# Performance work log

Measured on AMD Instinct MI355X. Metric: run time of the kernel, lower is better.

Reference implementation:

```python
import jax, jax.numpy as jnp
import numpy as np

L = 6        # gnn_layers
H = 4        # heads
C = 128      # per-head channels = hidden // heads
HID = 512    # hidden
IN = 768     # in_dim
N = 20000    # nodes
E = 320000   # edges
P = 100000   # scored pairs


def _gelu(v):
    return jax.nn.gelu(v, approximate=False)


def _ln(v, g, b):
    m = v.mean(-1, keepdims=True)
    var = v.var(-1, keepdims=True)
    return (v - m) / jnp.sqrt(var + 1e-5) * g + b


def setup_inputs() -> dict:
    key = jax.random.key(0)
    ks = jax.random.split(key, 24)
    g = lambda k, shape, s=0.02: (jax.random.normal(k, shape, jnp.float32) * s)
    inp = {}
    inp["x"] = jax.random.normal(ks[0], (N, IN), jnp.float32)
    inp["edge_index"] = jax.random.randint(ks[1], (2, E), 0, N)
    inp["edges"] = jax.random.randint(ks[2], (2, P), 0, N)
    # FeatureMixer (no alt branch)
    inp["mixer_W"] = g(ks[3], (IN, HID)); inp["mixer_b"] = jnp.zeros((HID,), jnp.float32)
    # Stacked TransformerConv params per layer
    inp["Wq"] = g(ks[4], (L, HID, HID)); inp["bq"] = jnp.zeros((L, HID), jnp.float32)
    inp["Wk"] = g(ks[5], (L, HID, HID)); inp["bk"] = jnp.zeros((L, HID), jnp.float32)
    inp["Wv"] = g(ks[6], (L, HID, HID)); inp["bv"] = jnp.zeros((L, HID), jnp.float32)
    inp["Ws"] = g(ks[7], (L, HID, HID)); inp["bs"] = jnp.zeros((L, HID), jnp.float32)  # lin_skip (root weight)
    inp["ln_g"] = jnp.ones((L, HID), jnp.float32); inp["ln_b"] = jnp.zeros((L, HID), jnp.float32)
    # Dual projections
    inp["syn_W"] = g(ks[8], (HID, HID)); inp["syn_b"] = jnp.zeros((HID,), jnp.float32)
    inp["ant_W"] = g(ks[9], (HID, HID)); inp["ant_b"] = jnp.zeros((HID,), jnp.float32)
    # Bilinear score matrices
    inp["W_syn"] = g(ks[10], (HID, HID), 0.04)
    inp["W_ant"] = g(ks[11], (HID, HID), 0.04)
    # Gate MLP: Linear(4*HID, HID) -> GELU -> Linear(HID, 1) -> Sigmoid
    inp["gW1"] = g(ks[12], (4 * HID, HID)); inp["gb1"] = jnp.zeros((HID,), jnp.float32)
    inp["gW2"] = g(ks[13], (HID, 1)); inp["gb2"] = jnp.zeros((1,), jnp.float32)
    return inp


def reference(x, edge_index, edges, mixer_W, mixer_b, Wq, bq, Wk, bk, Wv, bv,
              Ws, bs, ln_g, ln_b, syn_W, syn_b, ant_W, ant_b, W_syn, W_ant,
              gW1, gb1, gW2, gb2):
    src, dst = edge_index[0], edge_index[1]
    scale = 1.0 / np.sqrt(C).astype(np.float32)
    # FeatureMixer (eval mode: dropout = identity)
    h = _gelu(x @ mixer_W + mixer_b)  # [N, HID]
    for l in range(L):
        # node-side projections, then gather per edge
        q = (h @ Wq[l] + bq[l]).reshape(N, H, C)
        k = (h @ Wk[l] + bk[l]).reshape(N, H, C)
        v = (h @ Wv[l] + bv[l]).reshape(N, H, C)
        logits = (q[dst] * k[src]).sum(-1) * scale          # [E, H]
        mx = jax.ops.segment_max(logits, dst, num_segments=N)   # [N, H]
        ex = jnp.exp(logits - mx[dst])
        den = jax.ops.segment_sum(ex, dst, num_segments=N)      # [N, H]
        alpha = ex / den[dst]                                   # segment softmax over incoming edges
        msg = alpha[..., None] * v[src]                         # [E, H, C]
        out = jax.ops.segment_sum(msg, dst, num_segments=N).reshape(N, HID)
        out = out + h @ Ws[l] + bs[l]                           # root/skip term of TransformerConv
        out = _gelu(out)
        h = _ln(h + out, ln_g[l], ln_b[l])
    z_syn = _gelu(h @ syn_W + syn_b)
    z_ant = _gelu(h @ ant_W + ant_b)
    i, j = edges[0], edges[1]
    vi_s, vj_s = z_syn[i], z_syn[j]
    vi_a, vj_a = z_ant[i], z_ant[j]
    s_syn = ((vi_s @ W_syn) * vj_s).sum(-1)
    s_ant = ((vi_a @ W_ant) * vj_a).sum(-1)
    pair = jnp.concatenate([jnp.abs(vi_s - vj_s), vi_s * vj_s,
                            jnp.abs(vi_a - vj_a), vi_a * vj_a], axis=-1)  # [P, 4*HID]
    g = jax.nn.sigmoid(_gelu(pair @ gW1 + gb1) @ gW2 + gb2).squeeze(-1)
    return g * s_ant + (1.0 - g) * (-s_syn)
```

## Files before the change

kernel.cpp:

```cpp
#include <hip/hip_runtime.h>
#include <cstdint>

#define L_LAYERS 6

typedef __attribute__((ext_vector_type(8))) short bf16x8;
typedef __attribute__((ext_vector_type(4))) float f32x4;
typedef __attribute__((ext_vector_type(2))) float f32x2;

__device__ __forceinline__ float gelu1(float v) {
    return 0.5f * v * (1.0f + erff(v * 0.7071067811865475f));
}

__device__ __forceinline__ unsigned int f2bf2(float a, float b) {
    union { float f; unsigned u; } x, y;
    x.f = a; y.f = b;
    unsigned lo = (x.u + 0x7FFFu + ((x.u >> 16) & 1u)) >> 16;
    unsigned hi = (y.u + 0x7FFFu + ((y.u >> 16) & 1u)) & 0xFFFF0000u;
    return lo | hi;
}

__device__ __forceinline__ unsigned short f2bf1(float a) {
    union { float f; unsigned u; } x;
    x.f = a;
    return (unsigned short)((x.u + 0x7FFFu + ((x.u >> 16) & 1u)) >> 16);
}

__device__ __forceinline__ unsigned cvt_pk_bf16(float lo, float hi) {
    unsigned r;
    asm("v_cvt_pk_bf16_f32 %0, %1, %2" : "=v"(r) : "v"(lo), "v"(hi));
    return r;
}

__device__ __forceinline__ float2 bfp2(unsigned u) {
    union { unsigned u; float f; } a, b;
    a.u = u << 16;
    b.u = u & 0xFFFF0000u;
    return make_float2(a.f, b.f);
}

__device__ __forceinline__ void gload16(const void* g, void* l) {
    __builtin_amdgcn_global_load_lds(
        (const __attribute__((address_space(1))) void*)g,
        (__attribute__((address_space(3))) void*)l, 16, 0, 0);
}


__global__ void k_zero(int* __restrict__ p, int n) {
    int i = blockIdx.x * 256 + threadIdx.x;
    if (i < n) p[i] = 0;
}

__global__ void k_cvt(const float* __restrict__ x, short* __restrict__ xb, int n8) {
    int i = blockIdx.x * 256 + threadIdx.x;
    if (i < n8) {
        const float4* p = (const float4*)(x + (size_t)i * 8);
        float4 a0 = p[0], a1 = p[1];
        uint4 o;
        o.x = f2bf2(a0.x, a0.y);
        o.y = f2bf2(a0.z, a0.w);
        o.z = f2bf2(a1.x, a1.y);
        o.w = f2bf2(a1.z, a1.w);
        *(uint4*)(xb + (size_t)i * 8) = o;
    }
}


__global__ void k_hist(const int* __restrict__ dst, int* __restrict__ hist, int E) {
    int e = blockIdx.x * 256 + threadIdx.x;
    if (e < E) atomicAdd(&hist[dst[e]], 1);
}

__global__ __launch_bounds__(1024) void k_scan(const int* __restrict__ hist,
                                               int* __restrict__ off, int n) {
    __shared__ int buf[1024];
    __shared__ int carry;
    int tid = threadIdx.x;
    if (tid == 0) carry = 0;
    __syncthreads();
    for (int base = 0; base < n; base += 1024) {
        int v = (base + tid < n) ? hist[base + tid] : 0;
        buf[tid] = v;
        __syncthreads();
        int x = v;
        for (int o = 1; o < 1024; o <<= 1) {
            int t = (tid >= o) ? buf[tid - o] : 0;
            __syncthreads();
            x += t;
            buf[tid] = x;
            __syncthreads();
        }
        int c = carry;
        if (base + tid < n) off[base + tid] = c + x - v;
        __syncthreads();
        if (tid == 1023) carry = c + buf[1023];
        __syncthreads();
    }
    if (tid == 0) off[n] = carry;
}

__global__ void k_scatter(const int* __restrict__ src, const int* __restrict__ dst,
                          const int* __restrict__ off, int* __restrict__ cursor,
                          int* __restrict__ srcS, int E) {
    int e = blockIdx.x * 256 + threadIdx.x;
    if (e < E) {
        int d = dst[e];
        int pos = off[d] + atomicAdd(&cursor[d], 1);
        srcS[pos] = src[e];
    }
}


__global__ void k_wcat(const float* __restrict__ Wq, const float* __restrict__ Wk,
                       const float* __restrict__ Wv, const float* __restrict__ Ws,
                       short* __restrict__ Wt) {
    int idx = blockIdx.x * 256 + threadIdx.x;
    int k = idx & 511;
    int nf = (idx >> 9) & 2047;
    int l = idx >> 20;
    int sel = nf >> 9, nn = nf & 511;
    const float* W = (sel == 0) ? Wq : (sel == 1) ? Wk : (sel == 2) ? Wv : Ws;
    float v = W[((size_t)l * 512 + k) * 512 + nn];
    Wt[idx] = (short)f2bf1(v);
}

__global__ void k_tr(const float* __restrict__ W, short* __restrict__ Wt, int K, int N,
                     int swz) {
    int k = blockIdx.x * 256 + threadIdx.x;
    int n = blockIdx.y;
    if (k < K) {
        int kk = k;
        if (swz) kk = (k & ~31) | (((((k >> 3) & 3) ^ ((n >> 1) & 3))) << 3) | (k & 7);
        Wt[(size_t)n * K + kk] = (short)f2bf1(W[(size_t)k * N + n]);
    }
}

__global__ void k_bcat(const float* __restrict__ bq, const float* __restrict__ bk,
                       const float* __restrict__ bv, const float* __restrict__ bs,
                       float* __restrict__ bcat) {
    int idx = blockIdx.x * 256 + threadIdx.x;
    if (idx >= L_LAYERS * 2048) return;
    int l = idx >> 11, n = idx & 2047;
    int sel = n >> 9, nn = n & 511;
    const float* b = (sel == 0) ? bq : (sel == 1) ? bk : (sel == 2) ? bv : bs;
    bcat[idx] = b[l * 512 + nn];
}

__global__ void k_bdual(const float* __restrict__ sb, const float* __restrict__ ab,
                        float* __restrict__ bd) {
    int idx = blockIdx.x * 256 + threadIdx.x;
    if (idx < 1024) bd[idx] = (idx < 512) ? sb[idx] : ab[idx - 512];
}


__global__ __launch_bounds__(256) void gemm_bb(
    const short* __restrict__ A, int lda,
    const short* __restrict__ Bt,
    const float* __restrict__ bias,
    short* __restrict__ C, unsigned char* __restrict__ C8, float* __restrict__ Cf,
    int ldc, int M, int N, int K, int act, int asel) {
    __shared__ __align__(16) short As[3 * 128 * 32];
    __shared__ __align__(16) short Bs[3 * 128 * 32];
    const int tid = threadIdx.x;
    const int lane = tid & 63;
    const int wave = tid >> 6;
    const int wr = (wave >> 1) * 64;
    const int wc = (wave & 1) * 64;
    const int l16 = lane & 15;
    const int quad = lane >> 4;
    const int row0 = blockIdx.x * 128;
    const int col0 = blockIdx.y * 128;
    const int c0 = tid, c1 = tid + 256;
    const int r0 = c0 >> 2, kq0 = (c0 & 3) * 8;
    const int r1 = c1 >> 2, kq1 = (c1 & 3) * 8;
    int ga0 = row0 + r0; if (ga0 >= M) ga0 = M - 1;
    int ga1 = row0 + r1; if (ga1 >= M) ga1 = M - 1;
    const short* Ab = A + (asel ? (col0 & 512) : 0);
    const short* Ap0 = Ab + (size_t)ga0 * lda + kq0;
    const short* Ap1 = Ab + (size_t)ga1 * lda + kq1;
    const short* Bp0 = Bt + (size_t)(col0 + r0) * K + kq0;
    const short* Bp1 = Bt + (size_t)(col0 + r1) * K + kq1;

    f32x4 acc[4][4];
#pragma unroll
    for (int i = 0; i < 4; ++i)
#pragma unroll
        for (int j = 0; j < 4; ++j)
            acc[i][j] = f32x4{0.f, 0.f, 0.f, 0.f};

    const int nsteps = K >> 5;
    gload16(Ap0, &As[c0 * 8]);
    gload16(Ap1, &As[c1 * 8]);
    gload16(Bp0, &Bs[c0 * 8]);
    gload16(Bp1, &Bs[c1 * 8]);
    gload16(Ap0 + 32, &As[4096 + c0 * 8]);
    gload16(Ap1 + 32, &As[4096 + c1 * 8]);
    gload16(Bp0 + 32, &Bs[4096 + c0 * 8]);
    gload16(Bp1 + 32, &Bs[4096 + c1 * 8]);
    int cur = 0, nx2 = 2;
#pragma unroll 1
    for (int ks = 0; ks < nsteps - 1; ++ks) {
        asm volatile("s_waitcnt vmcnt(4)" ::: "memory");
        __builtin_amdgcn_s_barrier();
        if (ks + 2 < nsteps) {
            const int kb = (ks + 2) * 32;
            const int nb = nx2 * 4096;
            gload16(Ap0 + kb, &As[nb + c0 * 8]);
            gload16(Ap1 + kb, &As[nb + c1 * 8]);
            gload16(Bp0 + kb, &Bs[nb + c0 * 8]);
            gload16(Bp1 + kb, &Bs[nb + c1 * 8]);
        }
        const int cb = cur * 4096;
        bf16x8 af[4], bfr[4];
#pragma unroll
        for (int i = 0; i < 4; ++i)
            af[i] = *(const bf16x8*)&As[cb + (wr + i * 16 + l16) * 32 + quad * 8];
#pragma unroll
        for (int j = 0; j < 4; ++j)
            bfr[j] = *(const bf16x8*)&Bs[cb + (wc + j * 16 + l16) * 32 + quad * 8];
#pragma unroll
        for (int i = 0; i < 4; ++i)
#pragma unroll
            for (int j = 0; j < 4; ++j)
                acc[i][j] = __builtin_amdgcn_mfma_f32_16x16x32_bf16(af[i], bfr[j], acc[i][j], 0, 0, 0);
        cur = (cur == 2) ? 0 : cur + 1;
        nx2 = (nx2 == 2) ? 0 : nx2 + 1;
    }
    {
        asm volatile("s_waitcnt vmcnt(0)" ::: "memory");
        __builtin_amdgcn_s_barrier();
        const int cb = cur * 4096;
        bf16x8 af[4], bfr[4];
#pragma unroll
        for (int i = 0; i < 4; ++i)
            af[i] = *(const bf16x8*)&As[cb + (wr + i * 16 + l16) * 32 + quad * 8];
#pragma unroll
        for (int j = 0; j < 4; ++j)
            bfr[j] = *(const bf16x8*)&Bs[cb + (wc + j * 16 + l16) * 32 + quad * 8];
#pragma unroll
        for (int i = 0; i < 4; ++i)
#pragma unroll
            for (int j = 0; j < 4; ++j)
                acc[i][j] = __builtin_amdgcn_mfma_f32_16x16x32_bf16(af[i], bfr[j], acc[i][j], 0, 0, 0);
    }
#pragma unroll
    for (int i = 0; i < 4; ++i) {
        int rbase = row0 + wr + i * 16 + quad * 4;
#pragma unroll
        for (int j = 0; j < 4; ++j) {
            int c = col0 + wc + j * 16 + l16;
            float bv = bias ? bias[c] : 0.0f;
#pragma unroll
            for (int rg = 0; rg < 4; ++rg) {
                int gr = rbase + rg;
                if (gr < M) {
                    float v = acc[i][j][rg] + bv;
                    if (act) v = gelu1(v);
                    C[(size_t)gr * ldc + c] = (short)f2bf1(v);
                    if (C8) {
                        int r8 = __builtin_amdgcn_cvt_pk_fp8_f32(v, v, 0, false);
                        C8[(size_t)gr * ldc + c] = (unsigned char)(r8 & 0xFF);
                    }
                    if (Cf) Cf[(size_t)gr * ldc + c] = v;
                }
            }
        }
    }
}


__global__ __launch_bounds__(256) void gemm_qkvs(
    const short* __restrict__ A,
    const short* __restrict__ Bt,
    const float* __restrict__ bias,
    short* __restrict__ qvs,
    unsigned char* __restrict__ kv8,
    int M, int mtiles) {
    const int K = 512;
    const int id = blockIdx.x;
    const int xcd = id & 7;
    const int t = id >> 3;
    const int col_t = t & 15;
    const int row_t = (t >> 4) * 8 + xcd;
    if (row_t >= mtiles) return;
    const int row0 = row_t * 128;
    const int col0 = col_t * 128;
    __shared__ __align__(16) short As[3 * 128 * 32];
    __shared__ __align__(16) short Bs[3 * 128 * 32];
    const int tid = threadIdx.x;
    const int lane = tid & 63;
    const int wave = tid >> 6;
    const int wr = (wave >> 1) * 64;
    const int wc = (wave & 1) * 64;
    const int l16 = lane & 15;
    const int quad = lane >> 4;
    const int c0 = tid, c1 = tid + 256;
    const int r0 = c0 >> 2, kq0 = (c0 & 3) * 8;
    const int r1 = c1 >> 2, kq1 = (c1 & 3) * 8;
    int ga0 = row0 + r0; if (ga0 >= M) ga0 = M - 1;
    int ga1 = row0 + r1; if (ga1 >= M) ga1 = M - 1;
    const short* Ap0 = A + (size_t)ga0 * K + kq0;
    const short* Ap1 = A + (size_t)ga1 * K + kq1;
    const short* Bp0 = Bt + (size_t)(col0 + r0) * K + kq0;
    const short* Bp1 = Bt + (size_t)(col0 + r1) * K + kq1;

    f32x4 acc[4][4];
#pragma unroll
    for (int i = 0; i < 4; ++i)
#pragma unroll
        for (int j = 0; j < 4; ++j)
            acc[i][j] = f32x4{0.f, 0.f, 0.f, 0.f};

    gload16(Ap0, &As[c0 * 8]);
    gload16(Ap1, &As[c1 * 8]);
    gload16(Bp0, &Bs[c0 * 8]);
    gload16(Bp1, &Bs[c1 * 8]);
    gload16(Ap0 + 32, &As[4096 + c0 * 8]);
    gload16(Ap1 + 32, &As[4096 + c1 * 8]);
    gload16(Bp0 + 32, &Bs[4096 + c0 * 8]);
    gload16(Bp1 + 32, &Bs[4096 + c1 * 8]);
    int cur = 0, nx2 = 2;
#pragma unroll 1
    for (int ks = 0; ks < 15; ++ks) {
        asm volatile("s_waitcnt vmcnt(4)" ::: "memory");
        __builtin_amdgcn_s_barrier();
        if (ks + 2 < 16) {
            const int kb = (ks + 2) * 32;
            const int nb = nx2 * 4096;
            gload16(Ap0 + kb, &As[nb + c0 * 8]);
            gload16(Ap1 + kb, &As[nb + c1 * 8]);
            gload16(Bp0 + kb, &Bs[nb + c0 * 8]);
            gload16(Bp1 + kb, &Bs[nb + c1 * 8]);
        }
        const int cb = cur * 4096;
        bf16x8 af[4], bfr[4];
#pragma unroll
        for (int i = 0; i < 4; ++i)
            af[i] = *(const bf16x8*)&As[cb + (wr + i * 16 + l16) * 32 + quad * 8];
#pragma unroll
        for (int j = 0; j < 4; ++j)
            bfr[j] = *(const bf16x8*)&Bs[cb + (wc + j * 16 + l16) * 32 + quad * 8];
#pragma unroll
        for (int i = 0; i < 4; ++i)
#pragma unroll
            for (int j = 0; j < 4; ++j)
                acc[i][j] = __builtin_amdgcn_mfma_f32_16x16x32_bf16(af[i], bfr[j], acc[i][j], 0, 0, 0);
        cur = (cur == 2) ? 0 : cur + 1;
        nx2 = (nx2 == 2) ? 0 : nx2 + 1;
    }
    {
        asm volatile("s_waitcnt vmcnt(0)" ::: "memory");
        __builtin_amdgcn_s_barrier();
        const int cb = cur * 4096;
        bf16x8 af[4], bfr[4];
#pragma unroll
        for (int i = 0; i < 4; ++i)
            af[i] = *(const bf16x8*)&As[cb + (wr + i * 16 + l16) * 32 + quad * 8];
#pragma unroll
        for (int j = 0; j < 4; ++j)
            bfr[j] = *(const bf16x8*)&Bs[cb + (wc + j * 16 + l16) * 32 + quad * 8];
#pragma unroll
        for (int i = 0; i < 4; ++i)
#pragma unroll
            for (int j = 0; j < 4; ++j)
                acc[i][j] = __builtin_amdgcn_mfma_f32_16x16x32_bf16(af[i], bfr[j], acc[i][j], 0, 0, 0);
    }
#pragma unroll
    for (int i = 0; i < 4; ++i) {
        int rbase = row0 + wr + i * 16 + quad * 4;
#pragma unroll
        for (int j = 0; j < 4; ++j) {
            int c = col0 + wc + j * 16 + l16;
            int sec = c >> 9;
            int cc = c & 511;
            float bv = bias[c];
#pragma unroll
            for (int rg = 0; rg < 4; ++rg) {
                int gr = rbase + rg;
                if (gr < M) {
                    float v = acc[i][j][rg] + bv;
                    if (sec == 1 || sec == 2) {
                        int r8 = __builtin_amdgcn_cvt_pk_fp8_f32(v, v, 0, false);
                        int off = (sec == 1) ? cc : 512 + cc;
                        kv8[(size_t)gr * 1024 + off] = (unsigned char)(r8 & 0xFF);
                    } else {
                        int off = (sec == 0) ? cc : 512 + cc;
                        qvs[(size_t)gr * 1024 + off] = (short)f2bf1(v);
                    }
                }
            }
        }
    }
}


__global__ __launch_bounds__(512, 2) void gemm_gate(
    const unsigned char* __restrict__ z8,
    const int* __restrict__ pi, const int* __restrict__ pj, int P,
    const short* __restrict__ Bt,
    const float* __restrict__ gb1,
    const float* __restrict__ gW2,
    const float* __restrict__ gb2,
    const float* __restrict__ ssyn,
    const float* __restrict__ sant,
    float* __restrict__ out) {
    __shared__ __align__(16) short Bab[2 * 512 * 32];
    __shared__ __align__(16) short Bmu[2 * 512 * 32];
    __shared__ __align__(16) short Asab[128 * 32];
    __shared__ __align__(16) short Asmu[128 * 32];
    __shared__ int iArr[128];
    __shared__ int jArr[128];
    __shared__ float rowsum[128];
    const int row0 = blockIdx.x * 128;
    const int tid = threadIdx.x;
    const int lane = tid & 63;
    const int wave = tid >> 6;
    const int wm = wave >> 2;
    const int wn = wave & 3;
    const int l16 = lane & 15;
    const int quad = lane >> 4;
    const int arow = tid >> 2;
    const int aslot = tid & 3;
    const int qs = (quad ^ ((l16 >> 1) & 3)) * 8;
    const int awoff = arow * 32 + ((aslot ^ ((arow >> 1) & 3)) << 3);

    if (tid < 128) {
        int p = row0 + tid;
        int ok = (p < P);
        iArr[tid] = ok ? pi[p] : 0;
        jArr[tid] = ok ? pj[p] : 0;
        rowsum[tid] = 0.0f;
    }
    __syncthreads();
    const unsigned char* zi = z8 + (size_t)iArr[arow] * 1024 + aslot * 8;
    const unsigned char* zj = z8 + (size_t)jArr[arow] * 1024 + aslot * 8;
    const short* brow = Bt + (size_t)(tid >> 2) * 2048 + (tid & 3) * 8;

    f32x4 acc[4][8];
#pragma unroll
    for (int i = 0; i < 4; ++i)
#pragma unroll
        for (int j = 0; j < 8; ++j)
            acc[i][j] = f32x4{0.f, 0.f, 0.f, 0.f};

    auto CHB = [](int kc) { return ((kc >> 4) << 10) + ((kc & 15) << 5); };
    auto KOFF = [](int kc) { return ((kc >> 4) << 9) + ((kc & 15) << 5); };
    auto STAGE = [&](int kc, int mu, short* buf) {
        const short* src = brow + CHB(kc) + (mu ? 512 : 0);
#pragma unroll
        for (int g = 0; g < 4; ++g)
            gload16(src + (size_t)(g * 128) * 2048, buf + (g * 512 + tid) * 8);
    };
    auto CVT = [&](uint2 xu, uint2 yu, uint4& aa, uint4& am) {
        f32x2 x0 = __builtin_amdgcn_cvt_pk_f32_fp8((int)xu.x, false);
        f32x2 x1 = __builtin_amdgcn_cvt_pk_f32_fp8((int)xu.x, true);
        f32x2 x2 = __builtin_amdgcn_cvt_pk_f32_fp8((int)xu.y, false);
        f32x2 x3 = __builtin_amdgcn_cvt_pk_f32_fp8((int)xu.y, true);
        f32x2 y0 = __builtin_amdgcn_cvt_pk_f32_fp8((int)yu.x, false);
        f32x2 y1 = __builtin_amdgcn_cvt_pk_f32_fp8((int)yu.x, true);
        f32x2 y2 = __builtin_amdgcn_cvt_pk_f32_fp8((int)yu.y, false);
        f32x2 y3 = __builtin_amdgcn_cvt_pk_f32_fp8((int)yu.y, true);
        aa.x = cvt_pk_bf16(fabsf(x0.x - y0.x), fabsf(x0.y - y0.y));
        aa.y = cvt_pk_bf16(fabsf(x1.x - y1.x), fabsf(x1.y - y1.y));
        aa.z = cvt_pk_bf16(fabsf(x2.x - y2.x), fabsf(x2.y - y2.y));
        aa.w = cvt_pk_bf16(fabsf(x3.x - y3.x), fabsf(x3.y - y3.y));
        am.x = cvt_pk_bf16(x0.x * y0.x, x0.y * y0.y);
        am.y = cvt_pk_bf16(x1.x * y1.x, x1.y * y1.y);
        am.z = cvt_pk_bf16(x2.x * y2.x, x2.y * y2.y);
        am.w = cvt_pk_bf16(x3.x * y3.x, x3.y * y3.y);
    };
    auto MFMA_PHASE = [&](const short* As, const short* Bp) {
        bf16x8 af[4];
#pragma unroll
        for (int i = 0; i < 4; ++i)
            af[i] = *(const bf16x8*)&As[(wm * 64 + i * 16 + l16) * 32 + qs];
#pragma unroll
        for (int j = 0; j < 8; ++j) {
            bf16x8 bf = *(const bf16x8*)&Bp[(wn * 128 + j * 16 + l16) * 32 + qs];
#pragma unroll
            for (int i = 0; i < 4; ++i)
                acc[i][j] = __builtin_amdgcn_mfma_f32_16x16x32_bf16(af[i], bf, acc[i][j], 0, 0, 0);
        }
    };

    STAGE(0, 0, Bab);
    uint2 xu = *(const uint2*)zi;
    uint2 yu = *(const uint2*)zj;
    uint4 aa, am, am_hold;
    CVT(xu, yu, aa, am);
    *(uint4*)&Asab[awoff] = aa;
    am_hold = am;

#pragma unroll 1
    for (int kc = 0; kc < 31; ++kc) {
        const int cur = kc & 1;
        STAGE(kc, 1, Bmu + cur * 16384);
        uint2 xn = *(const uint2*)(zi + KOFF(kc + 1));
        uint2 yn = *(const uint2*)(zj + KOFF(kc + 1));
        asm volatile("s_waitcnt vmcnt(6) lgkmcnt(0)" ::: "memory");
        __builtin_amdgcn_s_barrier();
        MFMA_PHASE(Asab, Bab + cur * 16384);
        *(uint4*)&Asmu[awoff] = am_hold;
        STAGE(kc + 1, 0, Bab + (cur ^ 1) * 16384);
        CVT(xn, yn, aa, am);
        asm volatile("s_waitcnt vmcnt(4) lgkmcnt(0)" ::: "memory");
        __builtin_amdgcn_s_barrier();
        MFMA_PHASE(Asmu, Bmu + cur * 16384);
        *(uint4*)&Asab[awoff] = aa;
        am_hold = am;
    }
    STAGE(31, 1, Bmu + 16384);
    asm volatile("s_waitcnt vmcnt(4) lgkmcnt(0)" ::: "memory");
    __builtin_amdgcn_s_barrier();
    MFMA_PHASE(Asab, Bab + 16384);
    *(uint4*)&Asmu[awoff] = am_hold;
    asm volatile("s_waitcnt vmcnt(0) lgkmcnt(0)" ::: "memory");
    __builtin_amdgcn_s_barrier();
    MFMA_PHASE(Asmu, Bmu + 16384);

#pragma unroll
    for (int i = 0; i < 4; ++i) {
#pragma unroll
        for (int rg = 0; rg < 4; ++rg) {
            float partial = 0.f;
#pragma unroll
            for (int j = 0; j < 8; ++j) {
                int cc = wn * 128 + j * 16 + l16;
                partial += gelu1(acc[i][j][rg] + gb1[cc]) * gW2[cc];
            }
            partial += __shfl_xor(partial, 1);
            partial += __shfl_xor(partial, 2);
            partial += __shfl_xor(partial, 4);
            partial += __shfl_xor(partial, 8);
            if (l16 == 0)
                atomicAdd(&rowsum[wm * 64 + i * 16 + quad * 4 + rg], partial);
        }
    }
    __syncthreads();
    if (tid < 128) {
        int p = row0 + tid;
        if (p < P) {
            float s = 1.0f / (1.0f + __expf(-(rowsum[tid] + gb2[0])));
            out[p] = s * sant[p] - (1.0f - s) * ssyn[p];
        }
    }
}


__global__ __launch_bounds__(256) void k_attn(const short* __restrict__ qvs,
                                              const unsigned char* __restrict__ kv8,
                                              const int* __restrict__ srcS,
                                              const int* __restrict__ offs,
                                              float* __restrict__ h,
                                              short* __restrict__ h_bf,
                                              const float* __restrict__ lng,
                                              const float* __restrict__ lnb, int Nn) {
    const int tid = threadIdx.x;
    const int lane = tid & 63;
    const int wv = tid >> 6;
    const int n = blockIdx.x * 4 + wv;
    if (n >= Nn) return;
    const int st = offs[n], en = offs[n + 1];
    const size_t chOff = (size_t)lane * 8;

    uint4 qv = *(const uint4*)(qvs + (size_t)n * 1024 + chOff);
    float2 q0 = bfp2(qv.x), q1 = bfp2(qv.y), q2 = bfp2(qv.z), q3 = bfp2(qv.w);
    float acc[8];
#pragma unroll
    for (int i = 0; i < 8; ++i) acc[i] = 0.f;
    float m_l = -3.4e38f, l_l = 0.f;

    auto PROC = [&](uint2 kq, uint2 vq) {
        f32x2 k0 = __builtin_amdgcn_cvt_pk_f32_fp8((int)kq.x, false);
        f32x2 k1 = __builtin_amdgcn_cvt_pk_f32_fp8((int)kq.x, true);
        f32x2 k2 = __builtin_amdgcn_cvt_pk_f32_fp8((int)kq.y, false);
        f32x2 k3 = __builtin_amdgcn_cvt_pk_f32_fp8((int)kq.y, true);
        float d = q0.x * k0.x + q0.y * k0.y + q1.x * k1.x + q1.y * k1.y +
                  q2.x * k2.x + q2.y * k2.y + q3.x * k3.x + q3.y * k3.y;
        d += __shfl_xor(d, 1);
        d += __shfl_xor(d, 2);
        d += __shfl_xor(d, 4);
        d += __shfl_xor(d, 8);
        float lg = d * 0.08838834764831845f;
        float m_new = fmaxf(m_l, lg);
        float sc = __expf(m_l - m_new);
        float p = __expf(lg - m_new);
        l_l = l_l * sc + p;
        m_l = m_new;
        f32x2 v0 = __builtin_amdgcn_cvt_pk_f32_fp8((int)vq.x, false);
        f32x2 v1 = __builtin_amdgcn_cvt_pk_f32_fp8((int)vq.x, true);
        f32x2 v2 = __builtin_amdgcn_cvt_pk_f32_fp8((int)vq.y, false);
        f32x2 v3 = __builtin_amdgcn_cvt_pk_f32_fp8((int)vq.y, true);
        acc[0] = acc[0] * sc + p * v0.x; acc[1] = acc[1] * sc + p * v0.y;
        acc[2] = acc[2] * sc + p * v1.x; acc[3] = acc[3] * sc + p * v1.y;
        acc[4] = acc[4] * sc + p * v2.x; acc[5] = acc[5] * sc + p * v2.y;
        acc[6] = acc[6] * sc + p * v3.x; acc[7] = acc[7] * sc + p * v3.y;
    };

    for (int e0 = st; e0 < en; e0 += 64) {
        int cnt = min(64, en - e0);
        int myS = (lane < cnt) ? srcS[e0 + lane] : 0;
        int ei = 0;
        for (; ei + 8 <= cnt; ei += 8) {
            const unsigned char* rp[8];
#pragma unroll
            for (int u = 0; u < 8; ++u) {
                int s = __shfl(myS, ei + u);
                rp[u] = kv8 + (size_t)s * 1024 + chOff;
            }
            uint2 kk[8], vv[8];
#pragma unroll
            for (int u = 0; u < 8; ++u) {
                kk[u] = *(const uint2*)rp[u];
                vv[u] = *(const uint2*)(rp[u] + 512);
            }
#pragma unroll
            for (int u = 0; u < 8; ++u) PROC(kk[u], vv[u]);
        }
        for (; ei < cnt; ++ei) {
            int s = __shfl(myS, ei);
            const unsigned char* srow = kv8 + (size_t)s * 1024 + chOff;
            uint2 kq = *(const uint2*)srow;
            uint2 vq = *(const uint2*)(srow + 512);
            PROC(kq, vq);
        }
    }
    float rinv = (en > st) ? 1.0f / l_l : 0.f;
    uint4 su = *(const uint4*)(qvs + (size_t)n * 1024 + 512 + chOff);
    float2 s0 = bfp2(su.x), s1 = bfp2(su.y), s2 = bfp2(su.z), s3 = bfp2(su.w);
    float sv[8] = {s0.x, s0.y, s1.x, s1.y, s2.x, s2.y, s3.x, s3.y};
    const float* hp = h + (size_t)n * 512 + chOff;
    float4 h0 = *(const float4*)hp;
    float4 h1 = *(const float4*)(hp + 4);
    float hv[8] = {h0.x, h0.y, h0.z, h0.w, h1.x, h1.y, h1.z, h1.w};
    float r[8];
    float sum = 0.f, ssq = 0.f;
#pragma unroll
    for (int i = 0; i < 8; ++i) {
        r[i] = hv[i] + gelu1(acc[i] * rinv + sv[i]);
        sum += r[i];
        ssq += r[i] * r[i];
    }
    for (int o = 32; o; o >>= 1) {
        sum += __shfl_xor(sum, o);
        ssq += __shfl_xor(ssq, o);
    }
    float mean = sum * (1.0f / 512.0f);
    float var = ssq * (1.0f / 512.0f) - mean * mean;
    float inv = rsqrtf(var + 1e-5f);
    const float* gp = lng + chOff;
    const float* bp = lnb + chOff;
    float4 g0 = *(const float4*)gp, g1 = *(const float4*)(gp + 4);
    float4 b0 = *(const float4*)bp, b1 = *(const float4*)(bp + 4);
    float ga[8] = {g0.x, g0.y, g0.z, g0.w, g1.x, g1.y, g1.z, g1.w};
    float ba[8] = {b0.x, b0.y, b0.z, b0.w, b1.x, b1.y, b1.z, b1.w};
    float o8[8];
#pragma unroll
    for (int i = 0; i < 8; ++i) o8[i] = (r[i] - mean) * inv * ga[i] + ba[i];
    float* hw = h + (size_t)n * 512 + chOff;
    *(float4*)hw = make_float4(o8[0], o8[1], o8[2], o8[3]);
    *(float4*)(hw + 4) = make_float4(o8[4], o8[5], o8[6], o8[7]);
    uint4 ob;
    ob.x = f2bf2(o8[0], o8[1]);
    ob.y = f2bf2(o8[2], o8[3]);
    ob.z = f2bf2(o8[4], o8[5]);
    ob.w = f2bf2(o8[6], o8[7]);
    *(uint4*)(h_bf + (size_t)n * 512 + chOff) = ob;
}


__global__ __launch_bounds__(256) void k_pairscore(const short* __restrict__ z,
                                                   const short* __restrict__ t,
                                                   const int* __restrict__ pi,
                                                   const int* __restrict__ pj,
                                                   float* __restrict__ ssyn,
                                                   float* __restrict__ sant, int P) {
    int p = blockIdx.x * 4 + (threadIdx.x >> 6);
    if (p >= P) return;
    int lane = threadIdx.x & 63;
    int i = pi[p], j = pj[p];
    uint4 a = *(const uint4*)(t + (size_t)i * 1024 + lane * 8);
    uint4 b = *(const uint4*)(z + (size_t)j * 1024 + lane * 8);
    float2 a0 = bfp2(a.x), a1 = bfp2(a.y), a2 = bfp2(a.z), a3 = bfp2(a.w);
    float2 b0 = bfp2(b.x), b1 = bfp2(b.y), b2 = bfp2(b.z), b3 = bfp2(b.w);
    float ds = a0.x * b0.x + a0.y * b0.y + a1.x * b1.x + a1.y * b1.y +
               a2.x * b2.x + a2.y * b2.y + a3.x * b3.x + a3.y * b3.y;
    uint4 c = *(const uint4*)(t + (size_t)i * 1024 + 512 + lane * 8);
    uint4 d = *(const uint4*)(z + (size_t)j * 1024 + 512 + lane * 8);
    float2 c0 = bfp2(c.x), c1 = bfp2(c.y), c2 = bfp2(c.z), c3 = bfp2(c.w);
    float2 d0 = bfp2(d.x), d1 = bfp2(d.y), d2 = bfp2(d.z), d3 = bfp2(d.w);
    float da = c0.x * d0.x + c0.y * d0.y + c1.x * d1.x + c1.y * d1.y +
               c2.x * d2.x + c2.y * d2.y + c3.x * d3.x + c3.y * d3.y;
    for (int o = 32; o; o >>= 1) {
        ds += __shfl_xor(ds, o);
        da += __shfl_xor(da, o);
    }
    if (lane == 0) { ssyn[p] = ds; sant[p] = da; }
}


extern "C" void kernel_launch(void* const* d_in, const int* in_sizes, int n_in,
                              void* d_out, int out_size, void* d_ws, size_t ws_size,
                              hipStream_t stream) {
    const float* x = (const float*)d_in[0];
    const int* ei = (const int*)d_in[1];
    const int* pe = (const int*)d_in[2];
    const float* mixer_W = (const float*)d_in[3];
    const float* mixer_b = (const float*)d_in[4];
    const float* Wq = (const float*)d_in[5];
    const float* bq = (const float*)d_in[6];
    const float* Wk = (const float*)d_in[7];
    const float* bk = (const float*)d_in[8];
    const float* Wv = (const float*)d_in[9];
    const float* bv = (const float*)d_in[10];
    const float* Ws = (const float*)d_in[11];
    const float* bs = (const float*)d_in[12];
    const float* ln_g = (const float*)d_in[13];
    const float* ln_b = (const float*)d_in[14];
    const float* syn_W = (const float*)d_in[15];
    const float* syn_b = (const float*)d_in[16];
    const float* ant_W = (const float*)d_in[17];
    const float* ant_b = (const float*)d_in[18];
    const float* W_syn = (const float*)d_in[19];
    const float* W_ant = (const float*)d_in[20];
    const float* gW1 = (const float*)d_in[21];
    const float* gb1 = (const float*)d_in[22];
    const float* gW2 = (const float*)d_in[23];
    const float* gb2 = (const float*)d_in[24];
    float* out = (float*)d_out;

    const int Nn = in_sizes[0] / 768;
    const int E = in_sizes[1] / 2;
    const int P = in_sizes[2] / 2;

    char* w = (char*)d_ws;
    auto alloc = [&](size_t bytes) -> char* {
        char* p = w;
        w += (bytes + 255) & ~(size_t)255;
        return p;
    };
    float* h = (float*)alloc((size_t)Nn * 512 * 4);
    short* h_bf = (short*)alloc((size_t)Nn * 512 * 2);
    char* U = alloc((size_t)Nn * 2048 * 2);
    short* x_bf = (short*)U;
    short* qvs = (short*)U;
    unsigned char* kv8 = (unsigned char*)(U + (size_t)Nn * 1024 * 2);
    short* zB = (short*)U;
    short* tB = (short*)(U + (size_t)Nn * 1024 * 2);
    unsigned char* z8 = (unsigned char*)alloc((size_t)Nn * 1024);
    float* ssyn = (float*)alloc((size_t)P * 2 * 4);
    float* sant = ssyn + P;
    int* srcS = (int*)alloc((size_t)E * 4);
    int* hist = (int*)alloc((size_t)Nn * 2 * 4);
    int* cursor = hist + Nn;
    int* offs = (int*)alloc((size_t)(Nn + 1) * 4);
    short* mixWt = (short*)alloc((size_t)512 * 768 * 2);
    short* wcat = (short*)alloc((size_t)L_LAYERS * 2048 * 512 * 2);
    short* dualWt = (short*)alloc((size_t)1024 * 512 * 2);
    short* bilWt = (short*)alloc((size_t)1024 * 512 * 2);
    short* gw1t = (short*)alloc((size_t)512 * 2048 * 2);
    float* bcat = (float*)alloc((size_t)L_LAYERS * 2048 * 4);
    float* bdual = (float*)alloc((size_t)1024 * 4);

    k_zero<<<(2 * Nn + 255) / 256, 256, 0, stream>>>(hist, 2 * Nn);
    k_hist<<<(E + 255) / 256, 256, 0, stream>>>(ei + E, hist, E);
    k_scan<<<1, 1024, 0, stream>>>(hist, offs, Nn);
    k_scatter<<<(E + 255) / 256, 256, 0, stream>>>(ei, ei + E, offs, cursor, srcS, E);

    k_wcat<<<(L_LAYERS * 2048 * 512) / 256, 256, 0, stream>>>(Wq, Wk, Wv, Ws, wcat);
    k_tr<<<dim3(3, 512), 256, 0, stream>>>(mixer_W, mixWt, 768, 512, 0);
    k_tr<<<dim3(2, 512), 256, 0, stream>>>(syn_W, dualWt, 512, 512, 0);
    k_tr<<<dim3(2, 512), 256, 0, stream>>>(ant_W, dualWt + 512 * 512, 512, 512, 0);
    k_tr<<<dim3(2, 512), 256, 0, stream>>>(W_syn, bilWt, 512, 512, 0);
    k_tr<<<dim3(2, 512), 256, 0, stream>>>(W_ant, bilWt + 512 * 512, 512, 512, 0);
    k_tr<<<dim3(8, 512), 256, 0, stream>>>(gW1, gw1t, 2048, 512, 1);
    k_bcat<<<48, 256, 0, stream>>>(bq, bk, bv, bs, bcat);
    k_bdual<<<4, 256, 0, stream>>>(syn_b, ant_b, bdual);

    const int mtiles = (Nn + 127) / 128;
    k_cvt<<<(Nn * 768 / 8 + 255) / 256, 256, 0, stream>>>(x, x_bf, Nn * 768 / 8);
    gemm_bb<<<dim3(mtiles, 4), 256, 0, stream>>>(x_bf, 768, mixWt, mixer_b, h_bf,
                                                 nullptr, h, 512, Nn, 512, 768, 1, 0);

    const int qk_grid = ((mtiles + 7) / 8) * 8 * 16;
    for (int l = 0; l < L_LAYERS; ++l) {
        gemm_qkvs<<<qk_grid, 256, 0, stream>>>(h_bf, wcat + (size_t)l * 2048 * 512,
                                               bcat + l * 2048, qvs, kv8, Nn, mtiles);
        k_attn<<<(Nn + 3) / 4, 256, 0, stream>>>(qvs, kv8, srcS, offs, h, h_bf,
                                                 ln_g + l * 512, ln_b + l * 512, Nn);
    }

    gemm_bb<<<dim3(mtiles, 8), 256, 0, stream>>>(h_bf, 512, dualWt, bdual, zB, z8,
                                                 nullptr, 1024, Nn, 1024, 512, 1, 0);
    gemm_bb<<<dim3(mtiles, 8), 256, 0, stream>>>(zB, 1024, bilWt, nullptr, tB, nullptr,
                                                 nullptr, 1024, Nn, 1024, 512, 0, 1);

    k_pairscore<<<(P + 3) / 4, 256, 0, stream>>>(zB, tB, pe, pe + P, ssyn, sant, P);

    const int ptiles2 = (P + 127) / 128;
    gemm_gate<<<ptiles2, 512, 0, stream>>>(z8, pe, pe + P, P, gw1t, gb1, gW2,
                                           gb2, ssyn, sant, out);
}
```

Baseline: 1.616 ms.

## Fuse bilinear pair scoring into the gate GEMM kernel

Removes the separate pair-score kernel and computes the syn and ant bilinear dot products inside the gate GEMM main loop. Each thread loads matching 8-element bf16 slices of tB[i] and zB[j] alongside the fp8 gathers, accumulates partial dots, and reduces them across the four threads of a row at the end. This drops a kernel launch and the round trip of the intermediate score arrays through global memory, and lets the gathers overlap MFMA work. In exchange it adds two vector loads per K-step to the gate loop's memory pipeline and retunes the wait counts, which could stall the B-tile staging.

Measured after the change: 1.598 ms. About the same (-1.1%).

```diff
diff --git a/kernel.cpp b/kernel.cpp
--- a/kernel.cpp
+++ b/kernel.cpp
@@ -400,8 +400,8 @@
     const float* __restrict__ gb1,
     const float* __restrict__ gW2,
     const float* __restrict__ gb2,
-    const float* __restrict__ ssyn,
-    const float* __restrict__ sant,
+    const short* __restrict__ tB,
+    const short* __restrict__ zB,
     float* __restrict__ out) {
     __shared__ __align__(16) short Bab[2 * 512 * 32];
     __shared__ __align__(16) short Bmu[2 * 512 * 32];
@@ -410,6 +410,8 @@
     __shared__ int iArr[128];
     __shared__ int jArr[128];
     __shared__ float rowsum[128];
+    __shared__ float dsS[128];
+    __shared__ float daS[128];
     const int row0 = blockIdx.x * 128;
     const int tid = threadIdx.x;
     const int lane = tid & 63;
@@ -433,6 +435,8 @@
     __syncthreads();
     const unsigned char* zi = z8 + (size_t)iArr[arow] * 1024 + aslot * 8;
     const unsigned char* zj = z8 + (size_t)jArr[arow] * 1024 + aslot * 8;
+    const short* tbi = tB + (size_t)iArr[arow] * 1024 + aslot * 8;
+    const short* zbj = zB + (size_t)jArr[arow] * 1024 + aslot * 8;
     const short* brow = Bt + (size_t)(tid >> 2) * 2048 + (tid & 3) * 8;
 
     f32x4 acc[4][8];
@@ -468,6 +472,12 @@
         am.z = cvt_pk_bf16(x2.x * y2.x, x2.y * y2.y);
         am.w = cvt_pk_bf16(x3.x * y3.x, x3.y * y3.y);
     };
+    auto DOT8 = [&](uint4 tv, uint4 zv) -> float {
+        float2 t0 = bfp2(tv.x), t1 = bfp2(tv.y), t2 = bfp2(tv.z), t3 = bfp2(tv.w);
+        float2 p0 = bfp2(zv.x), p1 = bfp2(zv.y), p2 = bfp2(zv.z), p3 = bfp2(zv.w);
+        return t0.x * p0.x + t0.y * p0.y + t1.x * p1.x + t1.y * p1.y +
+               t2.x * p2.x + t2.y * p2.y + t3.x * p3.x + t3.y * p3.y;
+    };
     auto MFMA_PHASE = [&](const short* As, const short* Bp) {
         bf16x8 af[4];
 #pragma unroll
@@ -485,10 +495,13 @@
     STAGE(0, 0, Bab);
     uint2 xu = *(const uint2*)zi;
     uint2 yu = *(const uint2*)zj;
+    uint4 tu = *(const uint4*)tbi;
+    uint4 zu = *(const uint4*)zbj;
     uint4 aa, am, am_hold;
     CVT(xu, yu, aa, am);
     *(uint4*)&Asab[awoff] = aa;
     am_hold = am;
+    float ds = 0.f, da = 0.f;
 
 #pragma unroll 1
     for (int kc = 0; kc < 31; ++kc) {
@@ -496,19 +509,26 @@
         STAGE(kc, 1, Bmu + cur * 16384);
         uint2 xn = *(const uint2*)(zi + KOFF(kc + 1));
         uint2 yn = *(const uint2*)(zj + KOFF(kc + 1));
+        {
+            float pd = DOT8(tu, zu);
+            if (kc < 16) ds += pd; else da += pd;
+        }
         asm volatile("s_waitcnt vmcnt(6) lgkmcnt(0)" ::: "memory");
         __builtin_amdgcn_s_barrier();
         MFMA_PHASE(Asab, Bab + cur * 16384);
         *(uint4*)&Asmu[awoff] = am_hold;
         STAGE(kc + 1, 0, Bab + (cur ^ 1) * 16384);
+        tu = *(const uint4*)(tbi + KOFF(kc + 1));
+        zu = *(const uint4*)(zbj + KOFF(kc + 1));
         CVT(xn, yn, aa, am);
-        asm volatile("s_waitcnt vmcnt(4) lgkmcnt(0)" ::: "memory");
+        asm volatile("s_waitcnt vmcnt(6) lgkmcnt(0)" ::: "memory");
         __builtin_amdgcn_s_barrier();
         MFMA_PHASE(Asmu, Bmu + cur * 16384);
         *(uint4*)&Asab[awoff] = aa;
         am_hold = am;
     }
     STAGE(31, 1, Bmu + 16384);
+    da += DOT8(tu, zu);
     asm volatile("s_waitcnt vmcnt(4) lgkmcnt(0)" ::: "memory");
     __builtin_amdgcn_s_barrier();
     MFMA_PHASE(Asab, Bab + 16384);
@@ -516,6 +536,12 @@
     asm volatile("s_waitcnt vmcnt(0) lgkmcnt(0)" ::: "memory");
     __builtin_amdgcn_s_barrier();
     MFMA_PHASE(Asmu, Bmu + 16384);
+
+    ds += __shfl_xor(ds, 1);
+    ds += __shfl_xor(ds, 2);
+    da += __shfl_xor(da, 1);
+    da += __shfl_xor(da, 2);
+    if (aslot == 0) { dsS[arow] = ds; daS[arow] = da; }
 
 #pragma unroll
     for (int i = 0; i < 4; ++i) {
@@ -540,7 +566,7 @@
         int p = row0 + tid;
         if (p < P) {
             float s = 1.0f / (1.0f + __expf(-(rowsum[tid] + gb2[0])));
-            out[p] = s * sant[p] - (1.0f - s) * ssyn[p];
+            out[p] = s * daS[tid] - (1.0f - s) * dsS[tid];
         }
     }
 }
@@ -665,36 +691,6 @@
     ob.z = f2bf2(o8[4], o8[5]);
     ob.w = f2bf2(o8[6], o8[7]);
     *(uint4*)(h_bf + (size_t)n * 512 + chOff) = ob;
-}
-
-
-__global__ __launch_bounds__(256) void k_pairscore(const short* __restrict__ z,
-                                                   const short* __restrict__ t,
-                                                   const int* __restrict__ pi,
-                                                   const int* __restrict__ pj,
-                                                   float* __restrict__ ssyn,
-                                                   float* __restrict__ sant, int P) {
-    int p = blockIdx.x * 4 + (threadIdx.x >> 6);
-    if (p >= P) return;
-    int lane = threadIdx.x & 63;
-    int i = pi[p], j = pj[p];
-    uint4 a = *(const uint4*)(t + (size_t)i * 1024 + lane * 8);
-    uint4 b = *(const uint4*)(z + (size_t)j * 1024 + lane * 8);
-    float2 a0 = bfp2(a.x), a1 = bfp2(a.y), a2 = bfp2(a.z), a3 = bfp2(a.w);
-    float2 b0 = bfp2(b.x), b1 = bfp2(b.y), b2 = bfp2(b.z), b3 = bfp2(b.w);
-    float ds = a0.x * b0.x + a0.y * b0.y + a1.x * b1.x + a1.y * b1.y +
-               a2.x * b2.x + a2.y * b2.y + a3.x * b3.x + a3.y * b3.y;
-    uint4 c = *(const uint4*)(t + (size_t)i * 1024 + 512 + lane * 8);
-    uint4 d = *(const uint4*)(z + (size_t)j * 1024 + 512 + lane * 8);
-    float2 c0 = bfp2(c.x), c1 = bfp2(c.y), c2 = bfp2(c.z), c3 = bfp2(c.w);
-    float2 d0 = bfp2(d.x), d1 = bfp2(d.y), d2 = bfp2(d.z), d3 = bfp2(d.w);
-    float da = c0.x * d0.x + c0.y * d0.y + c1.x * d1.x + c1.y * d1.y +
-               c2.x * d2.x + c2.y * d2.y + c3.x * d3.x + c3.y * d3.y;
-    for (int o = 32; o; o >>= 1) {
-        ds += __shfl_xor(ds, o);
-        da += __shfl_xor(da, o);
-    }
-    if (lane == 0) { ssyn[p] = ds; sant[p] = da; }
 }
 
 
@@ -747,8 +743,6 @@
     short* zB = (short*)U;
     short* tB = (short*)(U + (size_t)Nn * 1024 * 2);
     unsigned char* z8 = (unsigned char*)alloc((size_t)Nn * 1024);
-    float* ssyn = (float*)alloc((size_t)P * 2 * 4);
-    float* sant = ssyn + P;
     int* srcS = (int*)alloc((size_t)E * 4);
     int* hist = (int*)alloc((size_t)Nn * 2 * 4);
     int* cursor = hist + Nn;
@@ -794,9 +788,7 @@
     gemm_bb<<<dim3(mtiles, 8), 256, 0, stream>>>(zB, 1024, bilWt, nullptr, tB, nullptr,
                                                  nullptr, 1024, Nn, 1024, 512, 0, 1);
 
-    k_pairscore<<<(P + 3) / 4, 256, 0, stream>>>(zB, tB, pe, pe + P, ssyn, sant, P);
-
     const int ptiles2 = (P + 127) / 128;
     gemm_gate<<<ptiles2, 512, 0, stream>>>(z8, pe, pe + P, P, gw1t, gb1, gW2,
-                                           gb2, ssyn, sant, out);
-}
+                                           gb2, tB, zB, out);
+}
```
